# Performance work log

Hardware: AMD Instinct MI355X
Metric: run time of the kernel (lower is better)

The kernel has to match this reference:

```python
import jax, jax.numpy as jnp
import numpy as np

B, S, D, H = 4, 2048, 512, 8
DEPTH = D // H


def setup_inputs() -> dict:
    key = jax.random.key(0)
    ks = jax.random.split(key, 12)
    scale = 0.02
    inp = {
        "q": jax.random.normal(ks[0], (B, S, D), dtype=jnp.float32),
        "k": jax.random.normal(ks[1], (B, S, D), dtype=jnp.float32),
        "v": jax.random.normal(ks[2], (B, S, D), dtype=jnp.float32),
        "mask": jax.random.randint(ks[3], (B, S, S), 0, 2, dtype=jnp.int32),
        "wq": jax.random.normal(ks[4], (D, D), dtype=jnp.float32) * scale,
        "bq": jnp.zeros((D,), dtype=jnp.float32),
        "wk": jax.random.normal(ks[5], (D, D), dtype=jnp.float32) * scale,
        "bk": jnp.zeros((D,), dtype=jnp.float32),
        "wv": jax.random.normal(ks[6], (D, D), dtype=jnp.float32) * scale,
        "bv": jnp.zeros((D,), dtype=jnp.float32),
        "wo": jax.random.normal(ks[7], (D, D), dtype=jnp.float32) * scale,
        "bo": jnp.zeros((D,), dtype=jnp.float32),
    }
    return inp


def _split_heads(x):
    # [B, S, D] -> [B, H, S, depth]
    b, s, _ = x.shape
    return x.reshape(b, s, H, DEPTH).transpose(0, 2, 1, 3)


def reference(q, k, v, mask, wq, bq, wk, bk, wv, bv, wo, bo):
    qh = _split_heads(q @ wq + bq)
    kh = _split_heads(k @ wk + bk)
    vh = _split_heads(v @ wv + bv)
    # scaled dot-product attention with additive mask, materializing [B,H,S,S]
    scores = jnp.einsum("bhqd,bhkd->bhqk", qh, kh) / jnp.sqrt(
        jnp.asarray(DEPTH, jnp.float32)
    )
    scores = scores + mask[:, None, :, :].astype(jnp.float32) * (-1e9)
    w = jax.nn.softmax(scores, axis=-1)
    o = jnp.einsum("bhqk,bhkd->bhqd", w, vh)
    o = o.transpose(0, 2, 1, 3).reshape(q.shape[0], -1, D)  # [B, S, D]
    return o @ wo + bo
```

## Files before the change

### kernel.cpp

```cpp
#include <hip/hip_runtime.h>
#include <hip/hip_bf16.h>
#include <stdint.h>

#define B_ 4
#define S_ 2048
#define D_ 512
#define H_ 8

typedef __attribute__((ext_vector_type(8))) short short8;
typedef __attribute__((ext_vector_type(4))) short short4v;
typedef __attribute__((ext_vector_type(4))) float f32x4;
typedef __attribute__((ext_vector_type(4))) unsigned short u16x4;

#define MFMA16(a,b,c) __builtin_amdgcn_mfma_f32_16x16x32_bf16((a),(b),(c),0,0,0)

#if __has_builtin(__builtin_amdgcn_mfma_f32_16x16x16bf16_1k)
#define HAVE16K 1
#define MFMA16K(a,b,c) __builtin_amdgcn_mfma_f32_16x16x16bf16_1k((a),(b),(c),0,0,0)
#else
#define HAVE16K 0
#endif

#if __has_builtin(__builtin_amdgcn_sbfe)
#define SBFE1(v, off) ((uint32_t)__builtin_amdgcn_sbfe((int)(v), (off), 1))
#else
#define SBFE1(v, off) ((uint32_t)(((int32_t)((v) << (31-(off)))) >> 31))
#endif

__device__ __forceinline__ unsigned short f2bf(float f){
    return __builtin_bit_cast(unsigned short, __float2bfloat16(f));
}

__device__ __forceinline__ float maskf(float p, uint32_t keep){
    return __builtin_bit_cast(float, __builtin_bit_cast(uint32_t, p) & keep);
}

__device__ __forceinline__ float max3f(float a, float b, float c){
    float d;
    asm("v_max3_f32 %0, %1, %2, %3" : "=v"(d) : "v"(a), "v"(b), "v"(c));
    return d;
}

__device__ __forceinline__ void gload_lds16(const void* g, void* l){
    __builtin_amdgcn_global_load_lds((const __attribute__((address_space(1))) uint32_t*)g,
                                     (__attribute__((address_space(3))) uint32_t*)l, 16, 0, 0);
}

__global__ __launch_bounds__(256) void prep_kernel(
    const int* __restrict__ mask, uint32_t* __restrict__ mout,
    const float* __restrict__ wq, const float* __restrict__ wk,
    const float* __restrict__ wv, const float* __restrict__ wo,
    unsigned short* __restrict__ wt)
{
    int bid = blockIdx.x;
    if (bid < 4096){
        int f = bid*256 + threadIdx.x;
        int mat = f >> 18;
        int rem = f & 262143;
        const float* Wm = (mat==0)?wq:(mat==1)?wk:(mat==2)?wv:wo;
        int kk = rem >> 9, nn = rem & 511;
        wt[(size_t)mat*262144 + (size_t)nn*512 + kk] = f2bf(Wm[rem]);
    } else {
        int idx = (bid-4096)*256 + threadIdx.x;
        const int4* p = (const int4*)(mask + (size_t)idx*32);
        uint32_t bits = 0;
        #pragma unroll
        for (int c=0;c<8;c++){
            int4 v = p[c];
            if (v.x) bits |= 1u << (c*4+0);
            if (v.y) bits |= 1u << (c*4+1);
            if (v.z) bits |= 1u << (c*4+2);
            if (v.w) bits |= 1u << (c*4+3);
        }
        mout[idx] = bits;
    }
}

__global__ __launch_bounds__(256) void proj_kernel(
    const float* __restrict__ q, const float* __restrict__ k, const float* __restrict__ v,
    const float* __restrict__ bq, const float* __restrict__ bk, const float* __restrict__ bv,
    const unsigned short* __restrict__ wt, unsigned short* __restrict__ outb)
{
    __shared__ uint8_t smem[32768];
    const int t = threadIdx.x, l = t&63, w = t>>6, g = l>>4, ln = l&15;
    const int z = blockIdx.z;
    const float* X = (z==0)? q : (z==1)? k : v;
    const float* bias = (z==0)? bq : (z==1)? bk : bv;
    const unsigned short* WTz = wt + (size_t)z*(D_*D_);
    unsigned short* out = outb + (size_t)z*((size_t)B_*H_*S_*64);
    const float scale = (z==0)? 0.18033688011112042f : 1.0f;
    const int m0 = blockIdx.x*128, n0 = blockIdx.y*128;
    uint8_t* As = smem; uint8_t* Bs = smem + 16384;
    const int RB = (w>>1)*64, CB = (w&1)*64;

    const f32x4 zz = {0.f,0.f,0.f,0.f};
    f32x4 acc[4][4];
    #pragma unroll
    for (int i=0;i<4;i++)
        #pragma unroll
        for (int j=0;j<4;j++) acc[i][j] = zz;

    for (int k0=0; k0<D_; k0+=64){
        __syncthreads();
        #pragma unroll
        for (int i=0;i<4;i++){
            int qc = w + i*4;
            int row = qc*8 + (l>>3);
            int colb = ((l&7)*16) ^ ((row&7)<<4);
            gload_lds16((const uint8_t*)WTz + (((size_t)(n0+row)*D_ + k0)<<1) + colb,
                        Bs + qc*1024);
        }
        #pragma unroll
        for (int i=0;i<4;i++){
            int c = t + i*256;
            int row = c>>3, cc = c&7;
            const float4* src = (const float4*)(X + (size_t)(m0+row)*D_ + k0 + cc*8);
            float4 u0 = src[0], u1 = src[1];
            uint32_t c0,c1,c2,c3;
            asm("v_cvt_pk_bf16_f32 %0, %1, %2" : "=v"(c0) : "v"(u0.x), "v"(u0.y));
            asm("v_cvt_pk_bf16_f32 %0, %1, %2" : "=v"(c1) : "v"(u0.z), "v"(u0.w));
            asm("v_cvt_pk_bf16_f32 %0, %1, %2" : "=v"(c2) : "v"(u1.x), "v"(u1.y));
            asm("v_cvt_pk_bf16_f32 %0, %1, %2" : "=v"(c3) : "v"(u1.z), "v"(u1.w));
            uint4 pk4; pk4.x=c0; pk4.y=c1; pk4.z=c2; pk4.w=c3;
            *(uint4*)(As + row*128 + ((cc*16) ^ ((row&7)<<4))) = pk4;
        }
        __syncthreads();
        #pragma unroll
        for (int kc=0; kc<2; kc++){
            short8 af[4], bfr[4];
            #pragma unroll
            for (int ai=0; ai<4; ai++){
                int row = RB + 16*ai + ln;
                af[ai] = *(const short8*)(As + row*128 + ((16*g + 64*kc) ^ ((row&7)<<4)));
            }
            #pragma unroll
            for (int bj=0; bj<4; bj++){
                int row = CB + 16*bj + ln;
                bfr[bj] = *(const short8*)(Bs + row*128 + ((16*g + 64*kc) ^ ((row&7)<<4)));
            }
            if (z == 2){
                #pragma unroll
                for (int ai=0; ai<4; ai++)
                    #pragma unroll
                    for (int bj=0; bj<4; bj++)
                        acc[ai][bj] = MFMA16(bfr[bj], af[ai], acc[ai][bj]);
            } else {
                #pragma unroll
                for (int ai=0; ai<4; ai++)
                    #pragma unroll
                    for (int bj=0; bj<4; bj++)
                        acc[ai][bj] = MFMA16(af[ai], bfr[bj], acc[ai][bj]);
            }
        }
    }

    if (z == 2){
        #pragma unroll
        for (int bj=0; bj<4; bj++){
            #pragma unroll
            for (int ai=0; ai<4; ai++){
                int s = m0 + RB + 16*ai + ln;
                #pragma unroll
                for (int r=0;r<4;r++){
                    int gn = n0 + CB + 16*bj + 4*g + r;
                    float val = acc[ai][bj][r] + bias[gn];
                    out[((size_t)(s>>11)*D_ + gn)*S_ + (s&2047)] = f2bf(val);
                }
            }
        }
    } else {
        #pragma unroll
        for (int bj=0; bj<4; bj++){
            int gn = n0 + CB + 16*bj + ln;
            float bv2 = bias[gn];
            int h = gn >> 6, dep = gn & 63;
            #pragma unroll
            for (int ai=0; ai<4; ai++){
                #pragma unroll
                for (int r=0;r<4;r++){
                    int gm = m0 + RB + 16*ai + 4*g + r;
                    float val = (acc[ai][bj][r] + bv2) * scale;
                    size_t o = ((size_t)(gm>>11)*H_ + h)*((size_t)S_*64) + (size_t)(gm&2047)*64 + dep;
                    out[o] = f2bf(val);
                }
            }
        }
    }
}

__global__ __launch_bounds__(256, 4) void attn_kernel(
    const unsigned short* __restrict__ qb, const unsigned short* __restrict__ kb,
    const unsigned short* __restrict__ vtb, const uint32_t* __restrict__ mb,
    unsigned short* __restrict__ ao)
{
#if HAVE16K
    __shared__ uint8_t smem[32768];
#else
    __shared__ uint8_t smem[40960];
#endif
    const int t = threadIdx.x, l = t&63, w = t>>6, g = l>>4, ln = l&15;
    const int fid = blockIdx.x + 32*blockIdx.y;
    const int slot = fid >> 3;
    const int bh = (fid & 7) + 8*(slot >> 5);
    const int q0 = (slot & 31) * 64;
    const int b = bh >> 3;
    const unsigned short* Q  = qb + (size_t)bh*((size_t)S_*64);
    const unsigned short* K  = kb + (size_t)bh*((size_t)S_*64);
    const unsigned short* VT = vtb + ((size_t)b*D_ + (bh&7)*64)*S_;

    const int qrow = q0 + 16*w + ln;
    const short8 qf0 = *(const short8*)(Q + (size_t)qrow*64 + 8*g);
    const short8 qf1 = *(const short8*)(Q + (size_t)qrow*64 + 8*g + 32);

    const int Msw = (ln&7)<<4;
    const int sw0 = (16*g) ^ Msw;
    const int sw1 = (16*g + 64) ^ Msw;
    uint8_t* kB0 = smem + ln*128 + sw0;
    uint8_t* kB1 = smem + ln*128 + sw1;
#if HAVE16K
    uint8_t* vB  = smem + 16384 + ln*128;
    const int vo0 = (8*g     ) ^ Msw;
    const int vo1 = (8*g + 32) ^ Msw;
    const int vo2 = (8*g + 64) ^ Msw;
    const int vo3 = (8*g + 96) ^ Msw;
#else
    uint8_t* Pw = smem + 32768 + w*2048;
    uint8_t* prd0 = Pw + ln*128 + sw0;
    uint8_t* prd1 = Pw + ln*128 + sw1;
#endif

    int krow0 = w*8 + (l>>3), krow1 = (w+4)*8 + (l>>3);
    int colb0 = ((l&7)*16) ^ ((krow0&7)<<4);
    int colb1 = ((l&7)*16) ^ ((krow1&7)<<4);
    int kof0 = krow0*128 + colb0,     kof1 = krow1*128 + colb1;
    int vof0 = krow0*(S_*2) + colb0,  vof1 = krow1*(S_*2) + colb1;
    const int ldo0 = w*1024, ldo1 = (w+4)*1024;

    const uint2* mptr = (const uint2*)(mb + ((size_t)b*S_ + qrow)*64);

    const f32x4 zz = {0.f,0.f,0.f,0.f};
    f32x4 O[4], O5 = zz;
    #pragma unroll
    for (int i=0;i<4;i++) O[i] = zz;
    float c = 0.f;

    const short4v onesv = {0x3F80,0x3F80,0x3F80,0x3F80};
#if !HAVE16K
    const short8 ones8 = {0x3F80,0x3F80,0x3F80,0x3F80,0x3F80,0x3F80,0x3F80,0x3F80};
#endif

    gload_lds16((const uint8_t*)K  + kof0, smem + ldo0);
    gload_lds16((const uint8_t*)K  + kof1, smem + ldo1);
    gload_lds16((const uint8_t*)VT + vof0, smem + 16384 + ldo0);
    gload_lds16((const uint8_t*)VT + vof1, smem + 16384 + ldo1);
    kof0 += 8192; kof1 += 8192; vof0 += 128; vof1 += 128;
    int curb = 0;
    uint2 mmc = mptr[0];

    for (int it=0; it<S_/64; ++it){
        __syncthreads();
        if (it < S_/64 - 1){
            int nx = curb ^ 8192;
            gload_lds16((const uint8_t*)K  + kof0, smem + nx + ldo0);
            gload_lds16((const uint8_t*)K  + kof1, smem + nx + ldo1);
            gload_lds16((const uint8_t*)VT + vof0, smem + 16384 + nx + ldo0);
            gload_lds16((const uint8_t*)VT + vof1, smem + 16384 + nx + ldo1);
            kof0 += 8192; kof1 += 8192; vof0 += 128; vof1 += 128;
        }
        uint2 mmn = mptr[(it+1)&31];
        const uint8_t* b0 = kB0 + curb;
        const uint8_t* b1 = kB1 + curb;

        f32x4 st[4];
        __builtin_amdgcn_s_setprio(1);
        #pragma unroll
        for (int t4=0;t4<4;t4++){
            short8 kf0 = *(const short8*)(b0 + 2048*t4);
            short8 kf1 = *(const short8*)(b1 + 2048*t4);
            st[t4] = MFMA16(kf0, qf0, zz);
            st[t4] = MFMA16(kf1, qf1, st[t4]);
        }
        __builtin_amdgcn_s_setprio(0);

        float m0a = max3f(st[0][0], st[0][1], st[0][2]);
        float m1a = max3f(st[0][3], st[1][0], st[1][1]);
        float m2a = max3f(st[1][2], st[1][3], st[2][0]);
        float m3a = max3f(st[2][1], st[2][2], st[2][3]);
        float m4a = max3f(st[3][0], st[3][1], st[3][2]);
        float lmax = fmaxf(max3f(m0a, m1a, m2a), max3f(m3a, m4a, st[3][3]));
        if (__builtin_expect(__any(lmax > c + 8.0f), 0)){
            float rm = lmax;
            rm = fmaxf(rm, __shfl_xor(rm, 16));
            rm = fmaxf(rm, __shfl_xor(rm, 32));
            float cnew = fmaxf(c, rm);
            float al = __builtin_amdgcn_exp2f(c - cnew);
            c = cnew;
            #pragma unroll
            for (int r=0;r<4;r++){
                float aO = __shfl(al, 4*g + r);
                #pragma unroll
                for (int db=0; db<4; db++) O[db][r] *= aO;
                O5[r] *= aO;
            }
        }

        uint32_t mi0 = (~mmc.x) >> (4*g);
        uint32_t mi1 = (~mmc.y) >> (4*g);
        short4v pa[4];
        auto genp = [&](float cc){
            #pragma unroll
            for (int t4=0;t4<4;t4++){
                uint32_t mi = (t4 >= 2) ? mi1 : mi0;
                const int base = (t4&1)*16;
                float p0 = maskf(__builtin_amdgcn_exp2f(st[t4][0] - cc), SBFE1(mi, base+0));
                float p1 = maskf(__builtin_amdgcn_exp2f(st[t4][1] - cc), SBFE1(mi, base+1));
                float p2 = maskf(__builtin_amdgcn_exp2f(st[t4][2] - cc), SBFE1(mi, base+2));
                float p3 = maskf(__builtin_amdgcn_exp2f(st[t4][3] - cc), SBFE1(mi, base+3));
                uint32_t lo, hi;
                asm("v_cvt_pk_bf16_f32 %0, %1, %2" : "=v"(lo) : "v"(p0), "v"(p1));
                asm("v_cvt_pk_bf16_f32 %0, %1, %2" : "=v"(hi) : "v"(p2), "v"(p3));
                uint2 u; u.x = lo; u.y = hi;
                pa[t4] = __builtin_bit_cast(short4v, u);
            }
        };
        if (__builtin_expect(__all(c == 0.0f), 1)) genp(0.0f); else genp(c);
        mmc = mmn;

#if HAVE16K
        __builtin_amdgcn_s_setprio(1);
        const uint8_t* vb = vB + curb;
        #pragma unroll
        for (int db=0; db<4; db++){
            short4v vf0 = *(const short4v*)(vb + 2048*db + vo0);
            short4v vf1 = *(const short4v*)(vb + 2048*db + vo1);
            short4v vf2 = *(const short4v*)(vb + 2048*db + vo2);
            short4v vf3 = *(const short4v*)(vb + 2048*db + vo3);
            O[db] = MFMA16K(pa[0], vf0, O[db]);
            O[db] = MFMA16K(pa[1], vf1, O[db]);
            O[db] = MFMA16K(pa[2], vf2, O[db]);
            O[db] = MFMA16K(pa[3], vf3, O[db]);
        }
        O5 = MFMA16K(pa[0], onesv, O5);
        O5 = MFMA16K(pa[1], onesv, O5);
        O5 = MFMA16K(pa[2], onesv, O5);
        O5 = MFMA16K(pa[3], onesv, O5);
        __builtin_amdgcn_s_setprio(0);
#else
        #pragma unroll
        for (int t4=0;t4<4;t4++){
            uint2 u = __builtin_bit_cast(uint2, pa[t4]);
            *(uint2*)(Pw + ln*128 + ((32*t4 + 8*g) ^ Msw)) = u;
        }
        asm volatile("s_waitcnt lgkmcnt(0)" ::: "memory");
        short8 pa0 = *(const short8*)prd0;
        short8 pa1 = *(const short8*)prd1;
        __builtin_amdgcn_s_setprio(1);
        #pragma unroll
        for (int db=0; db<4; db++){
            int dr = 16*db + ln;
            short8 vf0 = *(const short8*)(smem + 16384 + curb + dr*128 + ((16*g     ) ^ ((dr&7)<<4)));
            short8 vf1 = *(const short8*)(smem + 16384 + curb + dr*128 + ((16*g + 64) ^ ((dr&7)<<4)));
            O[db] = MFMA16(pa0, vf0, O[db]);
            O[db] = MFMA16(pa1, vf1, O[db]);
        }
        O5 = MFMA16(pa0, ones8, O5);
        O5 = MFMA16(pa1, ones8, O5);
        __builtin_amdgcn_s_setprio(0);
#endif
        curb ^= 8192;
    }

    #pragma unroll
    for (int r=0;r<4;r++){
        float inv = 1.0f / O5[r];
        int gm = b*S_ + q0 + 16*w + 4*g + r;
        #pragma unroll
        for (int db=0; db<4; db++){
            int col = (bh&7)*64 + 16*db + ln;
            ao[(size_t)gm*D_ + col] = f2bf(O[db][r]*inv);
        }
    }
}

__global__ __launch_bounds__(256) void outproj_kernel(
    const unsigned short* __restrict__ ao, const unsigned short* __restrict__ wt,
    const float* __restrict__ bo, float* __restrict__ out)
{
    __shared__ uint8_t smem[32768];
    const int t = threadIdx.x, l = t&63, w = t>>6, g = l>>4, ln = l&15;
    const unsigned short* WTz = wt + (size_t)3*(D_*D_);
    const int m0 = blockIdx.x*128, n0 = blockIdx.y*128;
    uint8_t* As = smem; uint8_t* Bs = smem + 16384;
    const int RB = (w>>1)*64, CB = (w&1)*64;

    const f32x4 zz = {0.f,0.f,0.f,0.f};
    f32x4 acc[4][4];
    #pragma unroll
    for (int i=0;i<4;i++)
        #pragma unroll
        for (int j=0;j<4;j++) acc[i][j] = zz;

    for (int k0=0; k0<D_; k0+=64){
        __syncthreads();
        #pragma unroll
        for (int i=0;i<4;i++){
            int qc = w + i*4;
            int row = qc*8 + (l>>3);
            int colb = ((l&7)*16) ^ ((row&7)<<4);
            gload_lds16((const uint8_t*)WTz + (((size_t)(n0+row)*D_ + k0)<<1) + colb,
                        Bs + qc*1024);
            gload_lds16((const uint8_t*)ao + (((size_t)(m0+row)*D_ + k0)<<1) + colb,
                        As + qc*1024);
        }
        __syncthreads();
        #pragma unroll
        for (int kc=0; kc<2; kc++){
            short8 af[4], bfr[4];
            #pragma unroll
            for (int ai=0; ai<4; ai++){
                int row = RB + 16*ai + ln;
                af[ai] = *(const short8*)(As + row*128 + ((16*g + 64*kc) ^ ((row&7)<<4)));
            }
            #pragma unroll
            for (int bj=0; bj<4; bj++){
                int row = CB + 16*bj + ln;
                bfr[bj] = *(const short8*)(Bs + row*128 + ((16*g + 64*kc) ^ ((row&7)<<4)));
            }
            #pragma unroll
            for (int ai=0; ai<4; ai++)
                #pragma unroll
                for (int bj=0; bj<4; bj++)
                    acc[ai][bj] = MFMA16(af[ai], bfr[bj], acc[ai][bj]);
        }
    }

    #pragma unroll
    for (int bj=0; bj<4; bj++){
        int gn = n0 + CB + 16*bj + ln;
        float bv2 = bo[gn];
        #pragma unroll
        for (int ai=0; ai<4; ai++){
            #pragma unroll
            for (int r=0;r<4;r++){
                int gm = m0 + RB + 16*ai + 4*g + r;
                out[(size_t)gm*D_ + gn] = acc[ai][bj][r] + bv2;
            }
        }
    }
}

extern "C" void kernel_launch(void* const* d_in, const int* in_sizes, int n_in,
                              void* d_out, int out_size, void* d_ws, size_t ws_size,
                              hipStream_t stream)
{
    const float* q  = (const float*)d_in[0];
    const float* k  = (const float*)d_in[1];
    const float* v  = (const float*)d_in[2];
    const int* mask = (const int*)d_in[3];
    const float* wq = (const float*)d_in[4];
    const float* bq = (const float*)d_in[5];
    const float* wk = (const float*)d_in[6];
    const float* bk = (const float*)d_in[7];
    const float* wv = (const float*)d_in[8];
    const float* bv = (const float*)d_in[9];
    const float* wo = (const float*)d_in[10];
    const float* bo = (const float*)d_in[11];

    uint8_t* ws = (uint8_t*)d_ws;
    unsigned short* qkvb = (unsigned short*)ws;
    unsigned short* ao   = (unsigned short*)(ws + 25165824);
    unsigned short* wt   = (unsigned short*)(ws + 33554432);
    uint32_t*       mb   = (uint32_t*)      (ws + 35651584);
    float* out = (float*)d_out;

    prep_kernel<<<dim3(6144), dim3(256), 0, stream>>>(mask, mb, wq, wk, wv, wo, wt);
    proj_kernel<<<dim3(64,4,3), dim3(256), 0, stream>>>(q, k, v, bq, bk, bv, wt, qkvb);
    attn_kernel<<<dim3(32,32), dim3(256), 0, stream>>>(qkvb, qkvb + 4194304, qkvb + 8388608, mb, ao);
    outproj_kernel<<<dim3(64,4), dim3(256), 0, stream>>>(ao, wt, bo, out);
}
```

Baseline: 123.8 us.

## Permute V-transpose sequence layout so attention reads 16-byte V fragments

The V projection writes its transposed output with a permuted sequence order within each 32-element chunk. The attention kernel can then load one 16-byte LDS vector per lane and split it into two 16x16x16 MFMA operands, instead of issuing four 8-byte reads. This halves LDS read instructions in the PV loop. The fallback path without the 16x16x16 bf16 MFMA builtin is removed, so the code now requires that builtin.

```diff
diff --git a/kernel.cpp b/kernel.cpp
--- a/kernel.cpp
+++ b/kernel.cpp
@@ -13,13 +13,7 @@
 typedef __attribute__((ext_vector_type(4))) unsigned short u16x4;
 
 #define MFMA16(a,b,c) __builtin_amdgcn_mfma_f32_16x16x32_bf16((a),(b),(c),0,0,0)
-
-#if __has_builtin(__builtin_amdgcn_mfma_f32_16x16x16bf16_1k)
-#define HAVE16K 1
 #define MFMA16K(a,b,c) __builtin_amdgcn_mfma_f32_16x16x16bf16_1k((a),(b),(c),0,0,0)
-#else
-#define HAVE16K 0
-#endif
 
 #if __has_builtin(__builtin_amdgcn_sbfe)
 #define SBFE1(v, off) ((uint32_t)__builtin_amdgcn_sbfe((int)(v), (off), 1))
@@ -155,16 +149,19 @@
     }
 
     if (z == 2){
+        const int lnperm = 8*(ln>>2) + (ln&3);
+        const int bidx = m0 >> 11;
+        const int schunk = (m0 + RB) & 2047;
         #pragma unroll
         for (int bj=0; bj<4; bj++){
             #pragma unroll
             for (int ai=0; ai<4; ai++){
-                int s = m0 + RB + 16*ai + ln;
+                int soff = schunk + 32*(ai>>1) + 4*(ai&1) + lnperm;
                 #pragma unroll
                 for (int r=0;r<4;r++){
                     int gn = n0 + CB + 16*bj + 4*g + r;
                     float val = acc[ai][bj][r] + bias[gn];
-                    out[((size_t)(s>>11)*D_ + gn)*S_ + (s&2047)] = f2bf(val);
+                    out[((size_t)bidx*D_ + gn)*S_ + soff] = f2bf(val);
                 }
             }
         }
@@ -193,11 +190,7 @@
     const unsigned short* __restrict__ vtb, const uint32_t* __restrict__ mb,
     unsigned short* __restrict__ ao)
 {
-#if HAVE16K
     __shared__ uint8_t smem[32768];
-#else
-    __shared__ uint8_t smem[40960];
-#endif
     const int t = threadIdx.x, l = t&63, w = t>>6, g = l>>4, ln = l&15;
     const int fid = blockIdx.x + 32*blockIdx.y;
     const int slot = fid >> 3;
@@ -217,17 +210,9 @@
     const int sw1 = (16*g + 64) ^ Msw;
     uint8_t* kB0 = smem + ln*128 + sw0;
     uint8_t* kB1 = smem + ln*128 + sw1;
-#if HAVE16K
     uint8_t* vB  = smem + 16384 + ln*128;
-    const int vo0 = (8*g     ) ^ Msw;
-    const int vo1 = (8*g + 32) ^ Msw;
-    const int vo2 = (8*g + 64) ^ Msw;
-    const int vo3 = (8*g + 96) ^ Msw;
-#else
-    uint8_t* Pw = smem + 32768 + w*2048;
-    uint8_t* prd0 = Pw + ln*128 + sw0;
-    uint8_t* prd1 = Pw + ln*128 + sw1;
-#endif
+    const int vpo0 = (16*g     ) ^ Msw;
+    const int vpo1 = (16*g + 64) ^ Msw;
 
     int krow0 = w*8 + (l>>3), krow1 = (w+4)*8 + (l>>3);
     int colb0 = ((l&7)*16) ^ ((krow0&7)<<4);
@@ -245,9 +230,6 @@
     float c = 0.f;
 
     const short4v onesv = {0x3F80,0x3F80,0x3F80,0x3F80};
-#if !HAVE16K
-    const short8 ones8 = {0x3F80,0x3F80,0x3F80,0x3F80,0x3F80,0x3F80,0x3F80,0x3F80};
-#endif
 
     gload_lds16((const uint8_t*)K  + kof0, smem + ldo0);
     gload_lds16((const uint8_t*)K  + kof1, smem + ldo1);
@@ -326,15 +308,16 @@
         if (__builtin_expect(__all(c == 0.0f), 1)) genp(0.0f); else genp(c);
         mmc = mmn;
 
-#if HAVE16K
         __builtin_amdgcn_s_setprio(1);
         const uint8_t* vb = vB + curb;
         #pragma unroll
         for (int db=0; db<4; db++){
-            short4v vf0 = *(const short4v*)(vb + 2048*db + vo0);
-            short4v vf1 = *(const short4v*)(vb + 2048*db + vo1);
-            short4v vf2 = *(const short4v*)(vb + 2048*db + vo2);
-            short4v vf3 = *(const short4v*)(vb + 2048*db + vo3);
+            short8 vp0 = *(const short8*)(vb + 2048*db + vpo0);
+            short8 vp1 = *(const short8*)(vb + 2048*db + vpo1);
+            short4v vf0 = {vp0[0],vp0[1],vp0[2],vp0[3]};
+            short4v vf1 = {vp0[4],vp0[5],vp0[6],vp0[7]};
+            short4v vf2 = {vp1[0],vp1[1],vp1[2],vp1[3]};
+            short4v vf3 = {vp1[4],vp1[5],vp1[6],vp1[7]};
             O[db] = MFMA16K(pa[0], vf0, O[db]);
             O[db] = MFMA16K(pa[1], vf1, O[db]);
             O[db] = MFMA16K(pa[2], vf2, O[db]);
@@ -345,28 +328,6 @@
         O5 = MFMA16K(pa[2], onesv, O5);
         O5 = MFMA16K(pa[3], onesv, O5);
         __builtin_amdgcn_s_setprio(0);
-#else
-        #pragma unroll
-        for (int t4=0;t4<4;t4++){
-            uint2 u = __builtin_bit_cast(uint2, pa[t4]);
-            *(uint2*)(Pw + ln*128 + ((32*t4 + 8*g) ^ Msw)) = u;
-        }
-        asm volatile("s_waitcnt lgkmcnt(0)" ::: "memory");
-        short8 pa0 = *(const short8*)prd0;
-        short8 pa1 = *(const short8*)prd1;
-        __builtin_amdgcn_s_setprio(1);
-        #pragma unroll
-        for (int db=0; db<4; db++){
-            int dr = 16*db + ln;
-            short8 vf0 = *(const short8*)(smem + 16384 + curb + dr*128 + ((16*g     ) ^ ((dr&7)<<4)));
-            short8 vf1 = *(const short8*)(smem + 16384 + curb + dr*128 + ((16*g + 64) ^ ((dr&7)<<4)));
-            O[db] = MFMA16(pa0, vf0, O[db]);
-            O[db] = MFMA16(pa1, vf1, O[db]);
-        }
-        O5 = MFMA16(pa0, ones8, O5);
-        O5 = MFMA16(pa1, ones8, O5);
-        __builtin_amdgcn_s_setprio(0);
-#endif
         curb ^= 8192;
     }
 
```

Measured after the change: 120.3 us. 2.9% less time.
